# Performance work log

Hardware: AMD Instinct MI355X
Metric: run time of the kernel (lower is better)

## Reference

```python
import jax, jax.numpy as jnp
import numpy as np

B, S, D = 4, 1024, 2048
H, KVH, HD = 32, 8, 64
N_REP = H // KVH  # 4
ROPE_THETA = 1000000.0


def _rope_tables(seq_len, head_dim, theta):
    inv_freq = 1.0 / (theta ** (np.arange(0, head_dim, 2, dtype=np.float32) / head_dim))
    t = np.arange(seq_len, dtype=np.float32)
    freqs = np.outer(t, inv_freq)                      # (S, HD/2)
    emb = np.concatenate([freqs, freqs], axis=-1)      # (S, HD)
    return jnp.asarray(np.cos(emb)), jnp.asarray(np.sin(emb))


def setup_inputs() -> dict:
    key = jax.random.key(0)
    kx, kq, kk, kv, ko = jax.random.split(key, 5)
    cos, sin = _rope_tables(S, HD, ROPE_THETA)
    s = 0.02
    return {
        "x": jax.random.normal(kx, (B, S, D), jnp.float32),
        "cos": cos,
        "sin": sin,
        "Wq": jax.random.normal(kq, (D, H * HD), jnp.float32) * s,
        "Wk": jax.random.normal(kk, (D, KVH * HD), jnp.float32) * s,
        "Wv": jax.random.normal(kv, (D, KVH * HD), jnp.float32) * s,
        "Wo": jax.random.normal(ko, (H * HD, D), jnp.float32) * s,
    }


def _rotate_half(t):
    t1, t2 = jnp.split(t, 2, axis=-1)
    return jnp.concatenate([-t2, t1], axis=-1)


def reference(x, cos, sin, Wq, Wk, Wv, Wo):
    # projections
    q = (x @ Wq).reshape(B, S, H, HD)      # (b, s, h, d)
    k = (x @ Wk).reshape(B, S, KVH, HD)
    v = (x @ Wv).reshape(B, S, KVH, HD)

    # RoPE: cos/sin (s, d) broadcast over heads (unsqueeze_dim=1 -> (s,1,d))
    c = cos[:, None, :]
    sn = sin[:, None, :]
    q = q * c + _rotate_half(q) * sn
    k = k * c + _rotate_half(k) * sn

    # GQA attention without physically repeating KV:
    # q grouped as (b, kvh, n_rep, s, d); repeat_kv '(h r)' maps q head g*n_rep+r -> kv head g
    qg = q.transpose(0, 2, 1, 3).reshape(B, KVH, N_REP, S, HD)
    kt = k.transpose(0, 2, 1, 3)  # (b, kvh, s, d)
    vt = v.transpose(0, 2, 1, 3)

    scale = 1.0 / jnp.sqrt(jnp.asarray(HD, x.dtype))
    scores = jnp.einsum('bgrqd,bgkd->bgrqk', qg, kt) * scale  # (b, kvh, rep, s, s)
    probs = jax.nn.softmax(scores, axis=-1)
    out = jnp.einsum('bgrqk,bgkd->bgrqd', probs, vt)           # (b, kvh, rep, s, d)

    out = out.reshape(B, H, S, HD).transpose(0, 2, 1, 3).reshape(B, S, H * HD)
    return out @ Wo
```

## Files before the change

### kernel.cpp

```cpp
#include <hip/hip_runtime.h>

typedef unsigned short u16;
typedef __attribute__((ext_vector_type(8))) __bf16 bf16x8;
typedef __attribute__((ext_vector_type(4))) _Float16 f16x4;
typedef __attribute__((ext_vector_type(8))) _Float16 f16x8;
typedef __attribute__((ext_vector_type(4))) float f32x4;

#define BB 4
#define SS 1024
#define DD 2048
#define HH 32
#define KVHN 8
#define HDIM 64

__device__ __forceinline__ u16 f2b(float f) {
    union { float f; unsigned u; } v; v.f = f;
    unsigned r = v.u + 0x7FFFu + ((v.u >> 16) & 1u);
    return (u16)(r >> 16);
}
__device__ __forceinline__ float b2f(u16 h) {
    union { unsigned u; float f; } v; v.u = ((unsigned)h) << 16; return v.f;
}

__device__ __forceinline__ f32x4 mfma16(bf16x8 a, bf16x8 b, f32x4 c) {
    return __builtin_amdgcn_mfma_f32_16x16x32_bf16(a, b, c, 0, 0, 0);
}
__device__ __forceinline__ f32x4 mfma16h(f16x8 a, f16x8 b, f32x4 c) {
    return __builtin_amdgcn_mfma_f32_16x16x32_f16(a, b, c, 0, 0, 0);
}

__device__ __forceinline__ void async_cp16(const void* g, void* l) {
    __builtin_amdgcn_global_load_lds((__attribute__((address_space(1))) void*)g,
                                     (__attribute__((address_space(3))) void*)l,
                                     16, 0, 0);
}

__device__ __forceinline__ void block_sync() {
    asm volatile("" ::: "memory");
    __builtin_amdgcn_s_barrier();
    asm volatile("" ::: "memory");
}

__device__ __forceinline__ f16x8 pack8_f16(const float* p) {
    union { unsigned u[4]; f16x8 v; } pu;
    pu.u[0] = __builtin_bit_cast(unsigned, __builtin_amdgcn_cvt_pkrtz(p[0], p[1]));
    pu.u[1] = __builtin_bit_cast(unsigned, __builtin_amdgcn_cvt_pkrtz(p[2], p[3]));
    pu.u[2] = __builtin_bit_cast(unsigned, __builtin_amdgcn_cvt_pkrtz(p[4], p[5]));
    pu.u[3] = __builtin_bit_cast(unsigned, __builtin_amdgcn_cvt_pkrtz(p[6], p[7]));
    return pu.v;
}

__global__ __launch_bounds__(256) void prep_kernel(const float* __restrict__ x,
                                                   const float* __restrict__ Wq,
                                                   const float* __restrict__ Wk,
                                                   const float* __restrict__ Wv,
                                                   const float* __restrict__ Wo,
                                                   u16* __restrict__ xb,
                                                   u16* __restrict__ Wqkvt,
                                                   u16* __restrict__ Wot) {
    __shared__ float tile[32][33];
    int z = blockIdx.z;
    int tid = threadIdx.x;
    if (z == 4) {
        int lb = blockIdx.y * 64 + blockIdx.x;
        int i = (lb * 256 + tid) * 8;
        float4 v0 = *(const float4*)(x + i);
        float4 v1 = *(const float4*)(x + i + 4);
        uint4 r;
        r.x = (unsigned)f2b(v0.x) | ((unsigned)f2b(v0.y) << 16);
        r.y = (unsigned)f2b(v0.z) | ((unsigned)f2b(v0.w) << 16);
        r.z = (unsigned)f2b(v1.x) | ((unsigned)f2b(v1.y) << 16);
        r.w = (unsigned)f2b(v1.z) | ((unsigned)f2b(v1.w) << 16);
        *(uint4*)(xb + i) = r;
        return;
    }
    const float* W = (z == 0) ? Wq : (z == 1) ? Wk : (z == 2) ? Wv : Wo;
    int N = (z == 1 || z == 2) ? 512 : 2048;
    int n_off = (z == 1) ? 2048 : (z == 2) ? 2560 : 0;
    u16* Wt = (z == 3) ? Wot : Wqkvt;
    int n0 = blockIdx.x * 32;
    if (n0 >= N) return;
    int k0 = blockIdx.y * 32;
    int nj = tid & 31;
    int ki = tid >> 5;
#pragma unroll
    for (int it = 0; it < 4; it++) {
        int kk = it * 8 + ki;
        tile[kk][nj] = W[(size_t)(k0 + kk) * N + n0 + nj];
    }
    __syncthreads();
    int kp = tid & 15;
    int nn8 = tid >> 4;
#pragma unroll
    for (int pass = 0; pass < 2; pass++) {
        int nn = pass * 16 + nn8;
        unsigned v = (unsigned)f2b(tile[kp * 2][nn]) |
                     ((unsigned)f2b(tile[kp * 2 + 1][nn]) << 16);
        *(unsigned*)&Wt[(size_t)(n0 + nn + n_off) * 2048 + k0 + kp * 2] = v;
    }
}

__global__ __launch_bounds__(512, 2) void gemm_qkv(const u16* __restrict__ A,
                                                   const u16* __restrict__ Bt,
                                                   u16* __restrict__ C) {
    __shared__ __align__(16) u16 Ls[2][32768];
    const int tid = threadIdx.x;
    const int lane = tid & 63;
    const int w = tid >> 6;

    const int bid = blockIdx.x;
    const int xcd = bid & 7;
    const int loc = bid >> 3;
    const int mt = (xcd & 3) * 4 + (loc & 3);
    const int nt = (xcd >> 2) * 6 + (loc >> 2);
    const int m0 = mt * 256;
    const int n0 = nt * 256;

    const int wm_h = w >> 2;
    const int wn = (w & 3) * 64;
    const int lr = lane & 15;
    const int lg = lane >> 4;

    const int sr = lane >> 3;
    const int sl = (lane & 7) ^ (sr & 7);
    const u16* pA = A + (size_t)(m0 + w * 8 + sr) * 2048 + sl * 8;
    const u16* pB = Bt + (size_t)(n0 + w * 8 + sr) * 2048 + sl * 8;

#define STA(buf_, h_, kt_)                                                               \
    {                                                                                    \
        async_cp16(pA + (size_t)((h_) * 128) * 2048 + (kt_) * 64, &Ls[buf_][(h_) * 8192 + w * 512]);            \
        async_cp16(pA + (size_t)((h_) * 128 + 64) * 2048 + (kt_) * 64, &Ls[buf_][(h_) * 8192 + 4096 + w * 512]); \
    }
#define STB(buf_, h_, kt_)                                                               \
    {                                                                                    \
        async_cp16(pB + (size_t)((h_) * 128) * 2048 + (kt_) * 64, &Ls[buf_][16384 + (h_) * 8192 + w * 512]);            \
        async_cp16(pB + (size_t)((h_) * 128 + 64) * 2048 + (kt_) * 64, &Ls[buf_][16384 + (h_) * 8192 + 4096 + w * 512]); \
    }

    f32x4 acc[8][4];
    const f32x4 zero4 = {0.f, 0.f, 0.f, 0.f};
#pragma unroll
    for (int i = 0; i < 8; i++)
#pragma unroll
        for (int j = 0; j < 4; j++) acc[i][j] = zero4;

    bf16x8 af[8], b0[4], b1[4];

#define LDA(mh_, buf_)                                                                   \
    _Pragma("unroll") for (int mi = 0; mi < 4; mi++) _Pragma("unroll") for (int ks = 0; ks < 2; ks++) { \
        int rh = (mh_) * 64 + mi * 16 + lr;                                              \
        af[mi * 2 + ks] = *(const bf16x8*)(&Ls[buf_][wm_h * 8192 + rh * 64 + (((ks * 4 + lg) ^ (lr & 7)) * 8)]); \
    }
#define LDB(dst_, nh_, buf_)                                                             \
    _Pragma("unroll") for (int ni = 0; ni < 2; ni++) _Pragma("unroll") for (int ks = 0; ks < 2; ks++) { \
        int rowb = wn + (nh_) * 32 + ni * 16 + lr;                                       \
        dst_[ni * 2 + ks] = *(const bf16x8*)(&Ls[buf_][16384 + (rowb >> 7) * 8192 + (rowb & 127) * 64 + (((ks * 4 + lg) ^ (lr & 7)) * 8)]); \
    }
#define QMM(mh_, nh_, bb_)                                                               \
    __builtin_amdgcn_s_setprio(1);                                                       \
    _Pragma("unroll") for (int mi = 0; mi < 4; mi++) _Pragma("unroll") for (int ni = 0; ni < 2; ni++) { \
        acc[(mh_) * 4 + mi][(nh_) * 2 + ni] = mfma16(af[mi * 2 + 0], bb_[ni * 2 + 0], acc[(mh_) * 4 + mi][(nh_) * 2 + ni]); \
        acc[(mh_) * 4 + mi][(nh_) * 2 + ni] = mfma16(af[mi * 2 + 1], bb_[ni * 2 + 1], acc[(mh_) * 4 + mi][(nh_) * 2 + ni]); \
    }                                                                                    \
    __builtin_amdgcn_s_setprio(0);
#define WAITLDS                                                                          \
    asm volatile("s_waitcnt lgkmcnt(0)" ::: "memory");                                   \
    __builtin_amdgcn_sched_barrier(0);

    STA(0, 0, 0); STA(0, 1, 0); STB(0, 0, 0); STB(0, 1, 0);
    STB(1, 0, 1); STB(1, 1, 1);
    asm volatile("s_waitcnt vmcnt(0)" ::: "memory");
    block_sync();

#pragma unroll 1
    for (int I = 0; I < 16; ++I) {
        const int tb = 2 * I + 1;
        const int ta2 = (2 * I + 2) & 31;
        const int tb2 = (2 * I + 3) & 31;

        LDA(0, 0); LDB(b0, 0, 0);
        STA(1, 0, tb);
        block_sync(); WAITLDS;
        QMM(0, 0, b0);
        block_sync();

        LDB(b1, 1, 0);
        STA(1, 1, tb);
        block_sync(); WAITLDS;
        QMM(0, 1, b1);
        block_sync();

        LDA(1, 0);
        STB(0, 0, ta2);
        block_sync(); WAITLDS;
        QMM(1, 1, b1);
        block_sync();

        STB(0, 1, ta2);
        block_sync(); WAITLDS;
        QMM(1, 0, b0);
        asm volatile("s_waitcnt vmcnt(4)" ::: "memory");
        block_sync();

        LDA(0, 1); LDB(b0, 0, 1);
        STA(0, 0, ta2);
        block_sync(); WAITLDS;
        QMM(0, 0, b0);
        block_sync();

        LDB(b1, 1, 1);
        STA(0, 1, ta2);
        block_sync(); WAITLDS;
        QMM(0, 1, b1);
        block_sync();

        LDA(1, 1);
        STB(1, 0, tb2);
        block_sync(); WAITLDS;
        QMM(1, 1, b1);
        block_sync();

        STB(1, 1, tb2);
        block_sync(); WAITLDS;
        QMM(1, 0, b0);
        asm volatile("s_waitcnt vmcnt(4)" ::: "memory");
        block_sync();
    }
    asm volatile("s_waitcnt vmcnt(0)" ::: "memory");

    const int lq = lg * 4;
    const int wm = wm_h * 128;
#pragma unroll
    for (int mi = 0; mi < 8; mi++)
#pragma unroll
        for (int ni = 0; ni < 4; ni++)
#pragma unroll
            for (int i = 0; i < 4; i++) {
                int r = m0 + wm + mi * 16 + lq + i;
                int c = n0 + wn + ni * 16 + lr;
                C[(size_t)r * 3072 + c] = f2b(acc[mi][ni][i]);
            }
#undef STA
#undef STB
#undef LDA
#undef LDB
#undef QMM
#undef WAITLDS
}

__global__ __launch_bounds__(512, 2) void gemm_out(const u16* __restrict__ A,
                                                   const u16* __restrict__ Bt,
                                                   float* __restrict__ C) {
    __shared__ __align__(16) u16 Ls[2][24576];
    const int tid = threadIdx.x;
    const int lane = tid & 63;
    const int w = tid >> 6;

    const int bid = blockIdx.x;
    const int xcd = bid & 7;
    const int loc = bid >> 3;
    const int mt = (xcd & 3) * 4 + (loc & 3);
    const int nt = (xcd >> 2) * 8 + (loc >> 2);
    const int m0 = mt * 256;
    const int n0 = nt * 128;

    const int wm = (w >> 1) * 64;
    const int wn = (w & 1) * 64;
    const int lr = lane & 15;
    const int lg = lane >> 4;

    const int row0 = tid >> 2;
    const int g = tid & 3;
    const int sg = g ^ ((row0 >> 1) & 3);
    const u16* pA0 = A + (size_t)(m0 + row0) * 2048 + sg * 8;
    const u16* pA1 = pA0 + (size_t)128 * 2048;
    const u16* pB0 = Bt + (size_t)(n0 + row0) * 2048 + sg * 8;

#define OSTA(buf_, ks_, T_)                                                     \
    {                                                                           \
        async_cp16(pA0 + (T_) * 64 + (ks_) * 32, &Ls[buf_][(ks_) * 8192 + w * 512]);        \
        async_cp16(pA1 + (T_) * 64 + (ks_) * 32, &Ls[buf_][(ks_) * 8192 + 4096 + w * 512]); \
    }
#define OSTB(buf_, ks_, T_)                                                     \
    {                                                                           \
        async_cp16(pB0 + (T_) * 64 + (ks_) * 32, &Ls[buf_][16384 + (ks_) * 4096 + w * 512]); \
    }

    f32x4 acc[4][4];
    const f32x4 zero4 = {0.f, 0.f, 0.f, 0.f};
#pragma unroll
    for (int i = 0; i < 4; i++)
#pragma unroll
        for (int j = 0; j < 4; j++) acc[i][j] = zero4;

    bf16x8 af[4], bfr[4];

#define OLDA(ks_)                                                               \
    _Pragma("unroll") for (int mi = 0; mi < 4; mi++) {                          \
        int r_ = wm + mi * 16 + lr;                                             \
        af[mi] = *(const bf16x8*)(&Ls[cur][(ks_) * 8192 + r_ * 32 + ((lg ^ ((r_ >> 1) & 3)) * 8)]); \
    }
#define OLDB(ks_)                                                               \
    _Pragma("unroll") for (int ni = 0; ni < 4; ni++) {                          \
        int r_ = wn + ni * 16 + lr;                                             \
        bfr[ni] = *(const bf16x8*)(&Ls[cur][16384 + (ks_) * 4096 + r_ * 32 + ((lg ^ ((r_ >> 1) & 3)) * 8)]); \
    }
#define OMM                                                                     \
    __builtin_amdgcn_s_setprio(1);                                              \
    _Pragma("unroll") for (int mi = 0; mi < 4; mi++) _Pragma("unroll") for (int ni = 0; ni < 4; ni++) { \
        acc[mi][ni] = mfma16(af[mi], bfr[ni], acc[mi][ni]);                     \
    }                                                                           \
    __builtin_amdgcn_s_setprio(0);
#define OWAITMM                                                                 \
    asm volatile("s_waitcnt lgkmcnt(0)" ::: "memory");                          \
    __builtin_amdgcn_sched_barrier(0);

    OSTA(0, 0, 0); OSTB(0, 0, 0); OSTA(0, 1, 0); OSTB(0, 1, 0);
    OSTA(1, 0, 1); OSTB(1, 0, 1);
    asm volatile("s_waitcnt vmcnt(3)" ::: "memory");
    block_sync();

#pragma unroll 2
    for (int T = 0; T < 32; ++T) {
        const int cur = T & 1;
        const int oth = cur ^ 1;
        const int Tp1 = (T + 1) & 31;
        const int Tp2 = (T + 2) & 31;

        OLDA(0); OLDB(0);
        OSTA(oth, 1, Tp1); OSTB(oth, 1, Tp1);
        block_sync(); OWAITMM;
        OMM;
        block_sync();

        OLDA(1); OLDB(1);
        OSTA(cur, 0, Tp2); OSTB(cur, 0, Tp2);
        block_sync(); OWAITMM;
        OMM;
        asm volatile("s_waitcnt vmcnt(3)" ::: "memory");
        block_sync();
    }
    asm volatile("s_waitcnt vmcnt(0)" ::: "memory");

    const int lq = lg * 4;
#pragma unroll
    for (int mi = 0; mi < 4; mi++)
#pragma unroll
        for (int ni = 0; ni < 4; ni++)
#pragma unroll
            for (int i = 0; i < 4; i++) {
                int r = m0 + wm + mi * 16 + lq + i;
                int c = n0 + wn + ni * 16 + lr;
                C[(size_t)r * 2048 + c] = acc[mi][ni][i];
            }
#undef OSTA
#undef OSTB
#undef OLDA
#undef OLDB
#undef OMM
#undef OWAITMM
}

__global__ __launch_bounds__(256) void ropevt_kernel(const u16* __restrict__ QKV,
                                                     const float* __restrict__ cosT,
                                                     const float* __restrict__ sinT,
                                                     u16* __restrict__ Qh,
                                                     u16* __restrict__ Kh,
                                                     u16* __restrict__ Vt) {
    __shared__ u16 tile[64][65];
    const int bid = blockIdx.x;
    const int tid = threadIdx.x;
    if (bid < 2560) {
        const float QSC = 0.125f * 1.44269504088896f;
        int idx = bid * 256 + tid;
        int t = idx >> 2;
        int dq = (idx & 3) * 8;
        int hh = t % 40;
        int row = t / 40;
        int s = row & (SS - 1);
        int b = row >> 10;
        float4 c0 = *(const float4*)(cosT + s * HDIM + dq);
        float4 c1 = *(const float4*)(cosT + s * HDIM + dq + 4);
        float4 s0 = *(const float4*)(sinT + s * HDIM + dq);
        float4 s1 = *(const float4*)(sinT + s * HDIM + dq + 4);
        float cv[8] = {c0.x, c0.y, c0.z, c0.w, c1.x, c1.y, c1.z, c1.w};
        float sv[8] = {s0.x, s0.y, s0.z, s0.w, s1.x, s1.y, s1.z, s1.w};
        const u16* src;
        u16* dst;
        float scale;
        if (hh < 32) {
            src = QKV + (size_t)row * 3072 + hh * 64 + dq;
            dst = Qh + ((size_t)(b * HH + hh) * SS + s) * 64 + dq;
            scale = QSC;
        } else {
            int g = hh - 32;
            src = QKV + (size_t)row * 3072 + 2048 + g * 64 + dq;
            int rr = s & 7;
            int kpos = (s & ~31) + ((rr >= 4) ? 16 : 0) + ((s >> 3) & 3) * 4 + (rr & 3);
            dst = Kh + ((size_t)(b * KVHN + g) * SS + kpos) * 64 + dq;
            scale = 1.0f;
        }
        uint4 x1u = *(const uint4*)(src);
        uint4 x2u = *(const uint4*)(src + 32);
        const u16* x1p = (const u16*)&x1u;
        const u16* x2p = (const u16*)&x2u;
        unsigned o1[4], o2[4];
#pragma unroll
        for (int i = 0; i < 4; i++) {
            float a0 = b2f(x1p[2 * i]),     b0v = b2f(x2p[2 * i]);
            float a1 = b2f(x1p[2 * i + 1]), b1v = b2f(x2p[2 * i + 1]);
            float r00 = (a0 * cv[2 * i] - b0v * sv[2 * i]) * scale;
            float r01 = (a1 * cv[2 * i + 1] - b1v * sv[2 * i + 1]) * scale;
            float r10 = (b0v * cv[2 * i] + a0 * sv[2 * i]) * scale;
            float r11 = (b1v * cv[2 * i + 1] + a1 * sv[2 * i + 1]) * scale;
            o1[i] = (unsigned)f2b(r00) | ((unsigned)f2b(r01) << 16);
            o2[i] = (unsigned)f2b(r10) | ((unsigned)f2b(r11) << 16);
        }
        *(uint4*)(dst) = make_uint4(o1[0], o1[1], o1[2], o1[3]);
        *(uint4*)(dst + 32) = make_uint4(o2[0], o2[1], o2[2], o2[3]);
        return;
    }
    int blk = bid - 2560;
    int st = blk & 15;
    int t2 = blk >> 4;
    int g = t2 & 7;
    int b = t2 >> 3;
    int cj = tid & 63;
    int ri = tid >> 6;
    const u16* src = QKV + ((size_t)(b * SS + st * 64)) * 3072 + 2560 + g * 64;
#pragma unroll
    for (int it = 0; it < 16; it++) {
        int s_i = it * 4 + ri;
        tile[s_i][cj] = src[(size_t)s_i * 3072 + cj];
    }
    __syncthreads();
    u16* dst = Vt + ((size_t)(b * KVHN + g) * HDIM) * SS + st * 64;
#pragma unroll
    for (int it = 0; it < 16; it++) {
        int hd_i = it * 4 + ri;
        _Float16 hv = (_Float16)b2f(tile[cj][hd_i]);
        union { _Float16 h; u16 u; } cv2; cv2.h = hv;
        dst[(size_t)hd_i * SS + cj] = cv2.u;
    }
}

__global__ __launch_bounds__(256, 2) void flash_kernel(const u16* __restrict__ Qh,
                                                       const u16* __restrict__ Kh,
                                                       const u16* __restrict__ Vt,
                                                       u16* __restrict__ Attn) {
    __shared__ __align__(16) u16 Kls[2][4096];
    __shared__ __align__(16) u16 Vls[2][4096];
    const int tid = threadIdx.x;
    const int lane = tid & 63;
    const int w = tid >> 6;
    const int bid = blockIdx.x;
    const int gbp = ((bid & 7) << 2) | ((bid >> 3) & 3);
    const int qt2 = bid >> 5;
    const int g = gbp & 7;
    const int b = gbp >> 3;
    const int h = g * 4 + w;
    const int lr = lane & 15;
    const int lg = lane >> 4;
    const int lk8 = lg * 8;
    const int lq = lg * 4;

    const u16* Qbase = Qh + ((size_t)(b * HH + h) * SS + qt2 * 64) * HDIM;
    bf16x8 qb[4][2];
#pragma unroll
    for (int j = 0; j < 4; j++) {
        qb[j][0] = *(const bf16x8*)(Qbase + (size_t)(j * 16 + lr) * HDIM + lk8);
        qb[j][1] = *(const bf16x8*)(Qbase + (size_t)(j * 16 + lr) * HDIM + 32 + lk8);
    }

    const u16* Kbase = Kh + (size_t)(b * KVHN + g) * SS * HDIM;
    const u16* Vbase = Vt + (size_t)(b * KVHN + g) * HDIM * SS;

    const int r0 = tid >> 3;
    const int c0 = tid & 7;

    const f32x4 zero4 = {0.f, 0.f, 0.f, 0.f};
    const f32x4 initS = {-4.f, -4.f, -4.f, -4.f};
    f32x4 o[4][4];
    float lsum[4] = {0.f, 0.f, 0.f, 0.f};
#pragma unroll
    for (int j = 0; j < 4; j++)
#pragma unroll
        for (int i = 0; i < 4; i++) o[j][i] = zero4;

#define STAGE(kt, p)                                                              \
    {                                                                             \
        _Pragma("unroll") for (int sh = 0; sh < 2; sh++) {                        \
            int rr = r0 + sh * 32;                                                \
            int cs = c0 ^ (rr & 7);                                              \
            async_cp16(Kbase + (size_t)((kt) + rr) * HDIM + cs * 8,               \
                       &Kls[p][sh * 2048 + w * 512]);                             \
            async_cp16(Vbase + (size_t)rr * SS + (kt) + cs * 8,                   \
                       &Vls[p][sh * 2048 + w * 512]);                             \
        }                                                                         \
    }

    STAGE(0, 0);
    __syncthreads();

    for (int t = 0; t < 16; t++) {
        const int p = t & 1;
        if (t < 15) STAGE((t + 1) * 64, p ^ 1);

#pragma unroll
        for (int c = 0; c < 2; c++) {
            f32x4 s[2][4];
#pragma unroll
            for (int halfi = 0; halfi < 2; halfi++) {
                const int R = c * 32 + halfi * 16 + lr;
                const u16* kr = &Kls[p][R * 64];
                bf16x8 kb0 = *(const bf16x8*)(kr + ((lg ^ (R & 7)) * 8));
                bf16x8 kb1 = *(const bf16x8*)(kr + (((4 + lg) ^ (R & 7)) * 8));
#pragma unroll
                for (int j = 0; j < 4; j++) {
                    f32x4 a = initS;
                    a = mfma16(kb0, qb[j][0], a);
                    a = mfma16(kb1, qb[j][1], a);
                    s[halfi][j] = a;
                }
            }

            f16x8 va[4];
#pragma unroll
            for (int hdt = 0; hdt < 4; hdt++) {
                const int R2 = hdt * 16 + lr;
                va[hdt] = *(const f16x8*)(&Vls[p][R2 * 64 + (((c * 4 + lg) ^ (R2 & 7)) * 8)]);
            }

#pragma unroll
            for (int j = 0; j < 4; j++) {
                float pv[8];
#pragma unroll
                for (int r = 0; r < 4; r++) {
                    pv[r] = __builtin_amdgcn_exp2f(s[0][j][r]);
                    pv[4 + r] = __builtin_amdgcn_exp2f(s[1][j][r]);
                }
                lsum[j] += ((pv[0] + pv[1]) + (pv[2] + pv[3])) +
                           ((pv[4] + pv[5]) + (pv[6] + pv[7]));
                f16x8 pb = pack8_f16(pv);
#pragma unroll
                for (int hdt = 0; hdt < 4; hdt++)
                    o[j][hdt] = mfma16h(va[hdt], pb, o[j][hdt]);
            }
        }
        __syncthreads();
    }

#pragma unroll
    for (int j = 0; j < 4; j++) {
        float su = lsum[j];
        su += __shfl_xor(su, 16);
        su += __shfl_xor(su, 32);
        float inv = 1.f / su;
        u16* Ob = Attn + ((size_t)(b * SS + qt2 * 64 + j * 16 + lr)) * 2048 + h * 64;
#pragma unroll
        for (int hdt = 0; hdt < 4; hdt++) {
            unsigned r0p = (unsigned)f2b(o[j][hdt][0] * inv) | ((unsigned)f2b(o[j][hdt][1] * inv) << 16);
            unsigned r1p = (unsigned)f2b(o[j][hdt][2] * inv) | ((unsigned)f2b(o[j][hdt][3] * inv) << 16);
            *(uint2*)(Ob + hdt * 16 + lq) = make_uint2(r0p, r1p);
        }
    }
}

extern "C" void kernel_launch(void* const* d_in, const int* in_sizes, int n_in,
                              void* d_out, int out_size, void* d_ws, size_t ws_size,
                              hipStream_t stream) {
    (void)in_sizes; (void)n_in; (void)out_size; (void)ws_size;
    const float* x = (const float*)d_in[0];
    const float* cosT = (const float*)d_in[1];
    const float* sinT = (const float*)d_in[2];
    const float* Wq = (const float*)d_in[3];
    const float* Wk = (const float*)d_in[4];
    const float* Wv = (const float*)d_in[5];
    const float* Wo = (const float*)d_in[6];
    float* out = (float*)d_out;

    char* ws = (char*)d_ws;
    u16* Xb    = (u16*)(ws);
    u16* Wqkvt = (u16*)(ws + 16777216);
    u16* Wot   = (u16*)(ws + 29360128);
    u16* QKV   = (u16*)(ws + 37748736);
    u16* Qh    = (u16*)(ws + 62914560);
    u16* Kh    = (u16*)(ws + 79691776);
    u16* Vt    = (u16*)(ws + 83886080);
    u16* Attn  = (u16*)(ws + 88080384);

    prep_kernel<<<dim3(64, 64, 5), 256, 0, stream>>>(x, Wq, Wk, Wv, Wo, Xb, Wqkvt, Wot);

    gemm_qkv<<<192, 512, 0, stream>>>(Xb, Wqkvt, QKV);

    ropevt_kernel<<<3072, 256, 0, stream>>>(QKV, cosT, sinT, Qh, Kh, Vt);

    flash_kernel<<<512, 256, 0, stream>>>(Qh, Kh, Vt, Attn);

    gemm_out<<<256, 512, 0, stream>>>(Attn, Wot, out);
}
```

Before: 260.4 us.

## Fuse RoPE and Q/K head layout into QKV GEMM epilogue

The QKV GEMM epilogue now applies RoPE (with the Q scale) and writes Q and K directly in per-head layout, using the fact that each wave's 64-column slice is exactly one head so the rotate-half pairs sit in the same registers. V is written as fp16 to a compact buffer, and the former rope kernel is reduced to a V-only transpose. This removes the full bf16 QKV round trip through memory and most of a kernel launch. In exchange the epilogue uses scalar 2-byte stores and per-row cos/sin loads, which may be less coalesced than before.

```diff
diff --git a/kernel.cpp b/kernel.cpp
--- a/kernel.cpp
+++ b/kernel.cpp
@@ -102,7 +102,11 @@
 
 __global__ __launch_bounds__(512, 2) void gemm_qkv(const u16* __restrict__ A,
                                                    const u16* __restrict__ Bt,
-                                                   u16* __restrict__ C) {
+                                                   const float* __restrict__ cosT,
+                                                   const float* __restrict__ sinT,
+                                                   u16* __restrict__ Qh,
+                                                   u16* __restrict__ Kh,
+                                                   u16* __restrict__ Vbuf) {
     __shared__ __align__(16) u16 Ls[2][32768];
     const int tid = threadIdx.x;
     const int lane = tid & 63;
@@ -230,16 +234,66 @@
 
     const int lq = lg * 4;
     const int wm = wm_h * 128;
-#pragma unroll
-    for (int mi = 0; mi < 8; mi++)
-#pragma unroll
-        for (int ni = 0; ni < 4; ni++)
+    const int hb = (n0 + wn) >> 6;
+
+    if (hb < 32) {
+        const float QSC = 0.125f * 1.44269504088896f;
+#pragma unroll
+        for (int mi = 0; mi < 8; mi++)
 #pragma unroll
             for (int i = 0; i < 4; i++) {
                 int r = m0 + wm + mi * 16 + lq + i;
-                int c = n0 + wn + ni * 16 + lr;
-                C[(size_t)r * 3072 + c] = f2b(acc[mi][ni][i]);
+                int s = r & (SS - 1);
+                int b = r >> 10;
+                const float* cb = cosT + s * HDIM;
+                const float* sb = sinT + s * HDIM;
+                u16* drow = Qh + ((size_t)(b * HH + hb) * SS + s) * HDIM;
+#pragma unroll
+                for (int p = 0; p < 2; p++) {
+                    int dlo = p * 16 + lr;
+                    float c = cb[dlo], sn = sb[dlo];
+                    float alo = acc[mi][p][i], ahi = acc[mi][p + 2][i];
+                    drow[dlo]      = f2b((alo * c - ahi * sn) * QSC);
+                    drow[dlo + 32] = f2b((ahi * c + alo * sn) * QSC);
+                }
             }
+    } else if (hb < 40) {
+        int g = hb - 32;
+#pragma unroll
+        for (int mi = 0; mi < 8; mi++)
+#pragma unroll
+            for (int i = 0; i < 4; i++) {
+                int r = m0 + wm + mi * 16 + lq + i;
+                int s = r & (SS - 1);
+                int b = r >> 10;
+                int rr = s & 7;
+                int kpos = (s & ~31) + ((rr >= 4) ? 16 : 0) + ((s >> 3) & 3) * 4 + (rr & 3);
+                const float* cb = cosT + s * HDIM;
+                const float* sb = sinT + s * HDIM;
+                u16* drow = Kh + ((size_t)(b * KVHN + g) * SS + kpos) * HDIM;
+#pragma unroll
+                for (int p = 0; p < 2; p++) {
+                    int dlo = p * 16 + lr;
+                    float c = cb[dlo], sn = sb[dlo];
+                    float alo = acc[mi][p][i], ahi = acc[mi][p + 2][i];
+                    drow[dlo]      = f2b(alo * c - ahi * sn);
+                    drow[dlo + 32] = f2b(ahi * c + alo * sn);
+                }
+            }
+    } else {
+        int cv0 = (n0 + wn) - 2560;
+#pragma unroll
+        for (int mi = 0; mi < 8; mi++)
+#pragma unroll
+            for (int ni = 0; ni < 4; ni++)
+#pragma unroll
+                for (int i = 0; i < 4; i++) {
+                    int r = m0 + wm + mi * 16 + lq + i;
+                    union { _Float16 h; u16 u; } cvu;
+                    cvu.h = (_Float16)acc[mi][ni][i];
+                    Vbuf[(size_t)r * 512 + cv0 + ni * 16 + lr] = cvu.u;
+                }
+    }
 #undef STA
 #undef STB
 #undef LDA
@@ -361,86 +415,29 @@
 #undef OWAITMM
 }
 
-__global__ __launch_bounds__(256) void ropevt_kernel(const u16* __restrict__ QKV,
-                                                     const float* __restrict__ cosT,
-                                                     const float* __restrict__ sinT,
-                                                     u16* __restrict__ Qh,
-                                                     u16* __restrict__ Kh,
+__global__ __launch_bounds__(256) void vtrans_kernel(const u16* __restrict__ Vbuf,
                                                      u16* __restrict__ Vt) {
     __shared__ u16 tile[64][65];
-    const int bid = blockIdx.x;
-    const int tid = threadIdx.x;
-    if (bid < 2560) {
-        const float QSC = 0.125f * 1.44269504088896f;
-        int idx = bid * 256 + tid;
-        int t = idx >> 2;
-        int dq = (idx & 3) * 8;
-        int hh = t % 40;
-        int row = t / 40;
-        int s = row & (SS - 1);
-        int b = row >> 10;
-        float4 c0 = *(const float4*)(cosT + s * HDIM + dq);
-        float4 c1 = *(const float4*)(cosT + s * HDIM + dq + 4);
-        float4 s0 = *(const float4*)(sinT + s * HDIM + dq);
-        float4 s1 = *(const float4*)(sinT + s * HDIM + dq + 4);
-        float cv[8] = {c0.x, c0.y, c0.z, c0.w, c1.x, c1.y, c1.z, c1.w};
-        float sv[8] = {s0.x, s0.y, s0.z, s0.w, s1.x, s1.y, s1.z, s1.w};
-        const u16* src;
-        u16* dst;
-        float scale;
-        if (hh < 32) {
-            src = QKV + (size_t)row * 3072 + hh * 64 + dq;
-            dst = Qh + ((size_t)(b * HH + hh) * SS + s) * 64 + dq;
-            scale = QSC;
-        } else {
-            int g = hh - 32;
-            src = QKV + (size_t)row * 3072 + 2048 + g * 64 + dq;
-            int rr = s & 7;
-            int kpos = (s & ~31) + ((rr >= 4) ? 16 : 0) + ((s >> 3) & 3) * 4 + (rr & 3);
-            dst = Kh + ((size_t)(b * KVHN + g) * SS + kpos) * 64 + dq;
-            scale = 1.0f;
-        }
-        uint4 x1u = *(const uint4*)(src);
-        uint4 x2u = *(const uint4*)(src + 32);
-        const u16* x1p = (const u16*)&x1u;
-        const u16* x2p = (const u16*)&x2u;
-        unsigned o1[4], o2[4];
-#pragma unroll
-        for (int i = 0; i < 4; i++) {
-            float a0 = b2f(x1p[2 * i]),     b0v = b2f(x2p[2 * i]);
-            float a1 = b2f(x1p[2 * i + 1]), b1v = b2f(x2p[2 * i + 1]);
-            float r00 = (a0 * cv[2 * i] - b0v * sv[2 * i]) * scale;
-            float r01 = (a1 * cv[2 * i + 1] - b1v * sv[2 * i + 1]) * scale;
-            float r10 = (b0v * cv[2 * i] + a0 * sv[2 * i]) * scale;
-            float r11 = (b1v * cv[2 * i + 1] + a1 * sv[2 * i + 1]) * scale;
-            o1[i] = (unsigned)f2b(r00) | ((unsigned)f2b(r01) << 16);
-            o2[i] = (unsigned)f2b(r10) | ((unsigned)f2b(r11) << 16);
-        }
-        *(uint4*)(dst) = make_uint4(o1[0], o1[1], o1[2], o1[3]);
-        *(uint4*)(dst + 32) = make_uint4(o2[0], o2[1], o2[2], o2[3]);
-        return;
-    }
-    int blk = bid - 2560;
+    int blk = blockIdx.x;
     int st = blk & 15;
     int t2 = blk >> 4;
     int g = t2 & 7;
     int b = t2 >> 3;
+    int tid = threadIdx.x;
     int cj = tid & 63;
     int ri = tid >> 6;
-    const u16* src = QKV + ((size_t)(b * SS + st * 64)) * 3072 + 2560 + g * 64;
+    const u16* src = Vbuf + ((size_t)(b * SS + st * 64)) * 512 + g * 64;
 #pragma unroll
     for (int it = 0; it < 16; it++) {
         int s_i = it * 4 + ri;
-        tile[s_i][cj] = src[(size_t)s_i * 3072 + cj];
+        tile[s_i][cj] = src[(size_t)s_i * 512 + cj];
     }
     __syncthreads();
     u16* dst = Vt + ((size_t)(b * KVHN + g) * HDIM) * SS + st * 64;
 #pragma unroll
     for (int it = 0; it < 16; it++) {
         int hd_i = it * 4 + ri;
-        _Float16 hv = (_Float16)b2f(tile[cj][hd_i]);
-        union { _Float16 h; u16 u; } cv2; cv2.h = hv;
-        dst[(size_t)hd_i * SS + cj] = cv2.u;
+        dst[(size_t)hd_i * SS + cj] = tile[cj][hd_i];
     }
 }
 
@@ -583,7 +580,7 @@
     u16* Xb    = (u16*)(ws);
     u16* Wqkvt = (u16*)(ws + 16777216);
     u16* Wot   = (u16*)(ws + 29360128);
-    u16* QKV   = (u16*)(ws + 37748736);
+    u16* Vbuf  = (u16*)(ws + 37748736);
     u16* Qh    = (u16*)(ws + 62914560);
     u16* Kh    = (u16*)(ws + 79691776);
     u16* Vt    = (u16*)(ws + 83886080);
@@ -591,9 +588,9 @@
 
     prep_kernel<<<dim3(64, 64, 5), 256, 0, stream>>>(x, Wq, Wk, Wv, Wo, Xb, Wqkvt, Wot);
 
-    gemm_qkv<<<192, 512, 0, stream>>>(Xb, Wqkvt, QKV);
-
-    ropevt_kernel<<<3072, 256, 0, stream>>>(QKV, cosT, sinT, Qh, Kh, Vt);
+    gemm_qkv<<<192, 512, 0, stream>>>(Xb, Wqkvt, cosT, sinT, Qh, Kh, Vbuf);
+
+    vtrans_kernel<<<512, 256, 0, stream>>>(Vbuf, Vt);
 
     flash_kernel<<<512, 256, 0, stream>>>(Qh, Kh, Vt, Attn);
 
```

Result: no change. 258.6 us (-0.7%).
